# Optimization experiments

Measured on AMD Instinct MI355X. Metric: run time of the kernel, lower is better.

The kernel has to match this reference:

```python
import jax, jax.numpy as jnp
import numpy as np
from jax import lax

EPS = 1e-5
DN = ('NCHW', 'OIHW', 'NCHW')


def binarize(x):
    # sign(x) with 0 -> +1, matching _STESign.forward
    return jnp.where(x >= 0, jnp.ones_like(x), -jnp.ones_like(x))


def batchnorm(x, g, b, m, v):
    # inference BatchNorm2d with running stats
    scale = (g / jnp.sqrt(v + EPS))[None, :, None, None]
    shift = (b - m * g / jnp.sqrt(v + EPS))[None, :, None, None]
    return x * scale + shift


def conv(x, w, stride):
    return lax.conv_general_dilated(x, w, (stride, stride), [(1, 1), (1, 1)],
                                    dimension_numbers=DN)


def setup_inputs() -> dict:
    key = jax.random.key(0)
    ks = jax.random.split(key, 24)
    d = {}
    d['x'] = jax.random.normal(ks[0], (32, 3, 224, 224), dtype=jnp.float32)
    d['conv1_w'] = jax.random.normal(ks[1], (32, 3, 3, 3), dtype=jnp.float32) * 0.1
    d['conv2_w'] = jax.random.normal(ks[2], (64, 32, 3, 3), dtype=jnp.float32) * 0.1
    d['conv3_w'] = jax.random.normal(ks[3], (128, 64, 3, 3), dtype=jnp.float32) * 0.1
    d['conv4_w'] = jax.random.normal(ks[4], (256, 128, 3, 3), dtype=jnp.float32) * 0.1
    for i, c in zip(range(1, 5), (32, 64, 128, 256)):
        base = 4 + (i - 1) * 4
        d[f'bn{i}_g'] = jax.random.uniform(ks[base + 1], (c,), dtype=jnp.float32) + 0.5
        d[f'bn{i}_b'] = jax.random.normal(ks[base + 2], (c,), dtype=jnp.float32) * 0.1
        d[f'bn{i}_m'] = jax.random.normal(ks[base + 3], (c,), dtype=jnp.float32) * 0.1
        d[f'bn{i}_v'] = jax.random.uniform(ks[base + 4], (c,), dtype=jnp.float32) + 0.5
    d['fc_w'] = jax.random.normal(ks[21], (2, 256), dtype=jnp.float32) * 0.05
    d['fc_b'] = jnp.zeros((2,), dtype=jnp.float32)
    return d


def reference(x, conv1_w, conv2_w, conv3_w, conv4_w,
              bn1_g, bn1_b, bn1_m, bn1_v,
              bn2_g, bn2_b, bn2_m, bn2_v,
              bn3_g, bn3_b, bn3_m, bn3_v,
              bn4_g, bn4_b, bn4_m, bn4_v,
              fc_w, fc_b):
    # conv1 (real) + bn1
    h = batchnorm(conv(x, conv1_w, 1), bn1_g, bn1_b, bn1_m, bn1_v)
    # BinarizeConv2d: binarize input and weight, then real conv
    h = binarize(batchnorm(conv(binarize(h), binarize(conv2_w), 2), bn2_g, bn2_b, bn2_m, bn2_v))
    h = binarize(batchnorm(conv(binarize(h), binarize(conv3_w), 2), bn3_g, bn3_b, bn3_m, bn3_v))
    h = binarize(batchnorm(conv(binarize(h), binarize(conv4_w), 2), bn4_g, bn4_b, bn4_m, bn4_v))
    # adaptive avg pool to 1x1 -> mean over H,W
    h = jnp.mean(h, axis=(2, 3))  # [B, 256]
    return h @ fc_w.T + fc_b
```

## Files before the change

kernel.cpp:

```cpp
#include <hip/hip_runtime.h>
#include <stdint.h>
#include <math.h>

#define OFF_S1     0
#define OFF_W1T    256
#define OFF_T2     3712
#define OFF_P2     3968
#define OFF_T3     4224
#define OFF_P3     4736
#define OFF_T4     5248
#define OFF_P4     6272
#define OFF_W2     7296
#define OFF_W3     9600
#define OFF_W4     18816
#define OFF_A1     55680
#define OFF_A2     6478208
#define OFF_A3     9689472
#define OFF_A4     11295104

static __device__ __forceinline__ float2 bnf(float g, float b, float m, float v) {
    float sc = __fdiv_rn(g, __fsqrt_rn(__fadd_rn(v, 1e-5f)));
    float sh = __fsub_rn(b, __fmul_rn(m, sc));
    return make_float2(sc, sh);
}
static __device__ __forceinline__ bool bnpos(float s, float2 p) {
    return __fadd_rn(__fmul_rn(s, p.x), p.y) >= 0.0f;
}
static __device__ __forceinline__ int find_T(int K, float2 p) {
    int lo = -K - 2, hi = K + 2;
    while (lo + 2 < hi) {
        int mid = ((lo + hi) >> 1) & ~1;
        if (bnpos((float)mid, p)) hi = mid; else lo = mid;
    }
    return hi;
}

__global__ __launch_bounds__(256) void k_prep(
    const float* __restrict__ w1, const float* __restrict__ w2,
    const float* __restrict__ w3, const float* __restrict__ w4,
    const float* g1, const float* b1, const float* m1, const float* v1,
    const float* g2, const float* b2, const float* m2, const float* v2,
    const float* g3, const float* b3, const float* m3, const float* v3,
    const float* g4, const float* b4, const float* m4, const float* v4,
    float2* __restrict__ S1, float* __restrict__ W1T,
    int* __restrict__ T2, int* __restrict__ P2,
    int* __restrict__ T3, int* __restrict__ P3,
    int* __restrict__ T4, int* __restrict__ P4,
    uint32_t* __restrict__ W2, uint64_t* __restrict__ W3, uint64_t* __restrict__ W4)
{
    int gtid = blockIdx.x * 256 + threadIdx.x;
    int wid  = gtid >> 6;
    int lane = gtid & 63;

    if (wid < 576) {
        int oc = wid / 9, t = wid - oc * 9;
        float v = (lane < 32) ? w2[oc * 288 + lane * 9 + t] : -1.0f;
        uint64_t m = __ballot(v >= 0.0f);
        if (lane == 0) W2[wid] = (uint32_t)m;
    } else if (wid < 1728) {
        int i = wid - 576;
        int oc = i / 9, t = i - oc * 9;
        float v = w3[oc * 576 + lane * 9 + t];
        uint64_t m = __ballot(v >= 0.0f);
        if (lane == 0) W3[i] = m;
    } else if (wid < 6336) {
        int i = wid - 1728;
        int oc = i / 18, rem = i - oc * 18;
        int t = rem >> 1, h = rem & 1;
        float v = w4[oc * 1152 + (h * 64 + lane) * 9 + t];
        uint64_t m = __ballot(v >= 0.0f);
        if (lane == 0) W4[i] = m;
    } else {
        int t = gtid - 405504;
        if (t < 864) {
            int k = t >> 5, oc = t & 31;
            W1T[t] = w1[oc * 27 + k];
        } else if (t < 896) {
            int c = t - 864;
            S1[c] = bnf(g1[c], b1[c], m1[c], v1[c]);
        } else if (t < 960) {
            int c = t - 896;
            int T = find_T(288, bnf(g2[c], b2[c], m2[c], v2[c]));
            T2[c] = T; P2[c] = (288 - T) >> 1;
        } else if (t < 1088) {
            int c = t - 960;
            int T = find_T(576, bnf(g3[c], b3[c], m3[c], v3[c]));
            T3[c] = T; P3[c] = (576 - T) >> 1;
        } else if (t < 1344) {
            int c = t - 1088;
            int T = find_T(1152, bnf(g4[c], b4[c], m4[c], v4[c]));
            T4[c] = T; P4[c] = (1152 - T) >> 1;
        }
    }
}

__global__ __launch_bounds__(256) void k_conv1(
    const float* __restrict__ x, const float* __restrict__ w1,
    const float2* __restrict__ S1g, uint32_t* __restrict__ A1)
{
    __shared__ float  wl[27 * 32];
    __shared__ float2 s1[32];
    int tid = threadIdx.x;
    for (int i = tid; i < 864; i += 256) {
        int k = i >> 5, oc = i & 31;
        wl[i] = w1[oc * 27 + k];
    }
    if (tid < 32) s1[tid] = S1g[tid];
    __syncthreads();

    int idx = blockIdx.x * 256 + tid;
    int xp = idx % 112;
    int t  = idx / 112;
    int y  = t % 224;
    int b  = t / 224;
    int xc = xp * 2;

    const float* xb = x + (size_t)b * 3 * 50176;
    float xin[3][3][4];
    if ((unsigned)(y - 1) < 222u && (unsigned)(xp - 1) < 110u) {
        #pragma unroll
        for (int ic = 0; ic < 3; ic++)
            #pragma unroll
            for (int ky = 0; ky < 3; ky++) {
                const float* rp = xb + ic * 50176 + (y - 1 + ky) * 224 + (xc - 1);
                #pragma unroll
                for (int cx = 0; cx < 4; cx++) xin[ic][ky][cx] = rp[cx];
            }
    } else {
        #pragma unroll
        for (int ic = 0; ic < 3; ic++)
            #pragma unroll
            for (int ky = 0; ky < 3; ky++)
                #pragma unroll
                for (int cx = 0; cx < 4; cx++) {
                    int iy = y - 1 + ky, ix = xc - 1 + cx;
                    float v = 0.0f;
                    if ((unsigned)iy < 224u && (unsigned)ix < 224u)
                        v = xb[ic * 50176 + iy * 224 + ix];
                    xin[ic][ky][cx] = v;
                }
    }

    float acc0[32], acc1[32];
    #pragma unroll
    for (int oc = 0; oc < 32; oc++) { acc0[oc] = 0.0f; acc1[oc] = 0.0f; }

    const float4* wl4 = (const float4*)wl;
    #pragma unroll
    for (int k = 0; k < 27; k++) {
        int ic = k / 9, r = (k % 9) / 3, c = k % 3;
        float a0 = xin[ic][r][c];
        float a1 = xin[ic][r][c + 1];
        #pragma unroll
        for (int g8 = 0; g8 < 8; g8++) {
            float4 w = wl4[k * 8 + g8];
            acc0[g8 * 4 + 0] = fmaf(a0, w.x, acc0[g8 * 4 + 0]);
            acc0[g8 * 4 + 1] = fmaf(a0, w.y, acc0[g8 * 4 + 1]);
            acc0[g8 * 4 + 2] = fmaf(a0, w.z, acc0[g8 * 4 + 2]);
            acc0[g8 * 4 + 3] = fmaf(a0, w.w, acc0[g8 * 4 + 3]);
            acc1[g8 * 4 + 0] = fmaf(a1, w.x, acc1[g8 * 4 + 0]);
            acc1[g8 * 4 + 1] = fmaf(a1, w.y, acc1[g8 * 4 + 1]);
            acc1[g8 * 4 + 2] = fmaf(a1, w.z, acc1[g8 * 4 + 2]);
            acc1[g8 * 4 + 3] = fmaf(a1, w.w, acc1[g8 * 4 + 3]);
        }
    }

    uint32_t bits0 = 0, bits1 = 0;
    #pragma unroll
    for (int oc = 0; oc < 32; oc++) {
        bits0 |= (uint32_t)bnpos(acc0[oc], s1[oc]) << oc;
        bits1 |= (uint32_t)bnpos(acc1[oc], s1[oc]) << oc;
    }
    uint2* dst = (uint2*)(A1 + (size_t)b * 50176 + y * 224 + xc);
    *dst = make_uint2(bits0, bits1);
}

#define C2_LW 114
#define C3_LW 57

template<unsigned VM>
static __device__ __forceinline__ bool pred2(const uint32_t (&w)[3][9], int j,
                                             const uint32_t (&wr)[9], int T) {
    int pc = 0;
    #pragma unroll
    for (int ky = 0; ky < 3; ky++)
        #pragma unroll
        for (int kx = 0; kx < 3; kx++) {
            int ti = ky * 3 + kx;
            if (VM & (1u << ti)) pc += __popc(w[ky][2 * j + kx] ^ wr[ti]);
        }
    constexpr int nv = __builtin_popcount(VM);
    return pc <= ((32 * nv - T) >> 1);
}

template<unsigned VM0, unsigned VM>
static __device__ __forceinline__ void group2(const uint32_t* lrow, int g,
        const uint32_t (&wr)[9], int T, uint64_t* dst, int lane) {
    uint32_t win[3][9];
    int c0 = 8 * g;
    #pragma unroll
    for (int r = 0; r < 3; r++) {
        const uint32_t* rp = lrow + r * C2_LW + c0;
        uint2 a0 = *(const uint2*)(rp);
        uint2 a1 = *(const uint2*)(rp + 2);
        uint2 a2 = *(const uint2*)(rp + 4);
        uint2 a3 = *(const uint2*)(rp + 6);
        win[r][0] = a0.x; win[r][1] = a0.y; win[r][2] = a1.x; win[r][3] = a1.y;
        win[r][4] = a2.x; win[r][5] = a2.y; win[r][6] = a3.x; win[r][7] = a3.y;
        win[r][8] = rp[8];
    }
    uint64_t b0 = __ballot(pred2<VM0>(win, 0, wr, T));
    uint64_t b1 = __ballot(pred2<VM >(win, 1, wr, T));
    uint64_t b2 = __ballot(pred2<VM >(win, 2, wr, T));
    uint64_t b3 = __ballot(pred2<VM >(win, 3, wr, T));
    if (lane == 0) {
        ulonglong2* d = (ulonglong2*)(dst + 4 * g);
        d[0] = make_ulonglong2(b0, b1);
        d[1] = make_ulonglong2(b2, b3);
    }
}

__global__ __launch_bounds__(256) void k_conv2(
    const uint32_t* __restrict__ A1, const uint32_t* __restrict__ W2g,
    const int* __restrict__ T2, uint64_t* __restrict__ A2)
{
    __shared__ uint32_t lds[9 * C2_LW];
    int bi = blockIdx.x;
    int b = bi / 56, rem = bi % 56;
    int oyq = rem >> 1, h = rem & 1;
    int xs = h * 56;
    int tid = threadIdx.x;
    const uint32_t* ap = A1 + (size_t)b * 50176;
    for (int i = tid; i < 9 * C2_LW; i += 256) {
        int r = i / C2_LW, c = i - r * C2_LW;
        int iy = oyq * 8 - 1 + r, ix = 2 * xs - 1 + c;
        uint32_t v = 0;
        if ((unsigned)iy < 224u && (unsigned)ix < 224u) v = ap[iy * 224 + ix];
        lds[i] = v;
    }
    __syncthreads();

    int w = tid >> 6, lane = tid & 63;
    int oy = oyq * 4 + w;
    uint32_t wr[9];
    #pragma unroll
    for (int ti = 0; ti < 9; ti++) wr[ti] = W2g[lane * 9 + ti];
    int T = T2[lane];
    const uint32_t* lrow = lds + 2 * w * C2_LW;
    uint64_t* dst = A2 + (size_t)b * 12544 + oy * 112 + xs;
    bool left = (xs == 0);

    if (oy == 0) {
        if (left) group2<0x1B0, 0x1F8>(lrow, 0, wr, T, dst, lane);
        else      group2<0x1F8, 0x1F8>(lrow, 0, wr, T, dst, lane);
        for (int g = 1; g < 14; g++) group2<0x1F8, 0x1F8>(lrow, g, wr, T, dst, lane);
    } else {
        if (left) group2<0x1B6, 0x1FF>(lrow, 0, wr, T, dst, lane);
        else      group2<0x1FF, 0x1FF>(lrow, 0, wr, T, dst, lane);
        for (int g = 1; g < 14; g++) group2<0x1FF, 0x1FF>(lrow, g, wr, T, dst, lane);
    }
}

template<unsigned VM>
static __device__ __forceinline__ bool pred3(const uint64_t (&w)[3][9], int j,
                                             const uint64_t (&wr)[9], int T) {
    int pc = 0;
    #pragma unroll
    for (int ky = 0; ky < 3; ky++)
        #pragma unroll
        for (int kx = 0; kx < 3; kx++) {
            int ti = ky * 3 + kx;
            if (VM & (1u << ti)) pc += __popcll(w[ky][2 * j + kx] ^ wr[ti]);
        }
    constexpr int nv = __builtin_popcount(VM);
    return pc <= ((64 * nv - T) >> 1);
}

template<unsigned VM0, unsigned VM>
static __device__ __forceinline__ void group3(const uint64_t* lrow, int g,
        const uint64_t (&wr)[9], int T, uint64_t* dst, int lane) {
    uint64_t win[3][9];
    int c0 = 8 * g;
    #pragma unroll
    for (int r = 0; r < 3; r++) {
        const uint64_t* rp = lrow + r * C3_LW + c0;
        ulonglong2 a0 = *(const ulonglong2*)(rp);
        ulonglong2 a1 = *(const ulonglong2*)(rp + 2);
        ulonglong2 a2 = *(const ulonglong2*)(rp + 4);
        ulonglong2 a3 = *(const ulonglong2*)(rp + 6);
        win[r][0] = a0.x; win[r][1] = a0.y; win[r][2] = a1.x; win[r][3] = a1.y;
        win[r][4] = a2.x; win[r][5] = a2.y; win[r][6] = a3.x; win[r][7] = a3.y;
        win[r][8] = rp[8];
    }
    uint64_t b0 = __ballot(pred3<VM0>(win, 0, wr, T));
    uint64_t b1 = __ballot(pred3<VM >(win, 1, wr, T));
    uint64_t b2 = __ballot(pred3<VM >(win, 2, wr, T));
    uint64_t b3 = __ballot(pred3<VM >(win, 3, wr, T));
    if (lane == 0) {
        ulonglong2* d = (ulonglong2*)(dst + 4 * g);
        d[0] = make_ulonglong2(b0, b1);
        d[1] = make_ulonglong2(b2, b3);
    }
}

__global__ __launch_bounds__(256) void k_conv3(
    const uint64_t* __restrict__ A2, const uint64_t* __restrict__ W3g,
    const int* __restrict__ T3, uint64_t* __restrict__ A3)
{
    __shared__ uint64_t lds[5 * C3_LW];
    int bi = blockIdx.x;
    int b = bi / 56, rem = bi % 56;
    int oyp = rem >> 1, h = rem & 1;
    int xs = h * 28;
    int tid = threadIdx.x;
    const uint64_t* ap = A2 + (size_t)b * 12544;
    for (int i = tid; i < 5 * C3_LW; i += 256) {
        int r = i / C3_LW, c = i - r * C3_LW;
        int iy = oyp * 4 - 1 + r, ix = 2 * xs - 1 + c;
        uint64_t v = 0;
        if ((unsigned)iy < 112u && (unsigned)ix < 112u) v = ap[iy * 112 + ix];
        lds[i] = v;
    }
    __syncthreads();

    int w = tid >> 6, lane = tid & 63;
    int oy = oyp * 2 + (w >> 1);
    int g  = w & 1;
    int oc = g * 64 + lane;
    uint64_t wr[9];
    #pragma unroll
    for (int ti = 0; ti < 9; ti++) wr[ti] = W3g[oc * 9 + ti];
    int T = T3[oc];
    const uint64_t* lrow = lds + 2 * (w >> 1) * C3_LW;
    uint64_t* dst = A3 + (size_t)g * 100352 + (size_t)b * 3136 + oy * 56 + xs;
    bool left = (xs == 0);

    if (oy == 0) {
        if (left) group3<0x1B0, 0x1F8>(lrow, 0, wr, T, dst, lane);
        else      group3<0x1F8, 0x1F8>(lrow, 0, wr, T, dst, lane);
        for (int gg = 1; gg < 7; gg++) group3<0x1F8, 0x1F8>(lrow, gg, wr, T, dst, lane);
    } else {
        if (left) group3<0x1B6, 0x1FF>(lrow, 0, wr, T, dst, lane);
        else      group3<0x1FF, 0x1FF>(lrow, 0, wr, T, dst, lane);
        for (int gg = 1; gg < 7; gg++) group3<0x1FF, 0x1FF>(lrow, gg, wr, T, dst, lane);
    }
}

template<unsigned VM>
static __device__ __forceinline__ bool pred4(const uint64_t (&w0)[3][5],
                                             const uint64_t (&w1)[3][5], int j,
                                             const ulonglong2 (&wr)[9], int T) {
    int pc = 0;
    #pragma unroll
    for (int ky = 0; ky < 3; ky++)
        #pragma unroll
        for (int kx = 0; kx < 3; kx++) {
            int ti = ky * 3 + kx;
            if (VM & (1u << ti)) {
                pc += __popcll(w0[ky][2 * j + kx] ^ wr[ti].x);
                pc += __popcll(w1[ky][2 * j + kx] ^ wr[ti].y);
            }
        }
    constexpr int nv = __builtin_popcount(VM);
    return pc <= ((128 * nv - T) >> 1);
}

template<unsigned VM0, unsigned VM>
static __device__ __forceinline__ void group4(const uint64_t* ldsb, int g,
        const ulonglong2 (&wr)[9], int T, uint64_t* dst, int lane) {
    uint64_t w0[3][5], w1[3][5];
    int c0 = 4 * g;
    #pragma unroll
    for (int r = 0; r < 3; r++) {
        const uint64_t* rp0 = ldsb + r * 30 + c0;
        const uint64_t* rp1 = ldsb + (3 + r) * 30 + c0;
        ulonglong2 a0 = *(const ulonglong2*)(rp0);
        ulonglong2 a1 = *(const ulonglong2*)(rp0 + 2);
        w0[r][0] = a0.x; w0[r][1] = a0.y; w0[r][2] = a1.x; w0[r][3] = a1.y;
        w0[r][4] = rp0[4];
        ulonglong2 b0 = *(const ulonglong2*)(rp1);
        ulonglong2 b1 = *(const ulonglong2*)(rp1 + 2);
        w1[r][0] = b0.x; w1[r][1] = b0.y; w1[r][2] = b1.x; w1[r][3] = b1.y;
        w1[r][4] = rp1[4];
    }
    uint64_t r0 = __ballot(pred4<VM0>(w0, w1, 0, wr, T));
    uint64_t r1 = __ballot(pred4<VM >(w0, w1, 1, wr, T));
    if (lane == 0)
        *(ulonglong2*)(dst + 2 * g) = make_ulonglong2(r0, r1);
}

__global__ __launch_bounds__(256) void k_conv4(
    const uint64_t* __restrict__ A3, const uint64_t* __restrict__ W4g,
    const int* __restrict__ T4, uint64_t* __restrict__ A4)
{
    __shared__ uint64_t lds[2 * 3 * 30];
    int bi = blockIdx.x;
    int b = bi / 56, rem = bi % 56;
    int oy = rem >> 1, h = rem & 1;
    int xs = h * 14;
    int tid = threadIdx.x;
    const uint64_t* ap = A3 + (size_t)b * 3136;
    for (int i = tid; i < 174; i += 256) {
        int p = i / 87, j = i - p * 87;
        int r = j / 29, c = j - r * 29;
        int iy = 2 * oy - 1 + r, ix = 2 * xs - 1 + c;
        uint64_t v = 0;
        if ((unsigned)iy < 56u && (unsigned)ix < 56u)
            v = ap[(size_t)p * 100352 + iy * 56 + ix];
        lds[(p * 3 + r) * 30 + c] = v;
    }
    __syncthreads();

    int w = tid >> 6, lane = tid & 63;
    int oc = w * 64 + lane;
    ulonglong2 wr[9];
    const ulonglong2* wp = (const ulonglong2*)(W4g + oc * 18);
    #pragma unroll
    for (int ti = 0; ti < 9; ti++) wr[ti] = wp[ti];
    int T = T4[oc];
    uint64_t* dst = A4 + (size_t)w * 25088 + (size_t)b * 784 + oy * 28 + xs;
    bool left = (xs == 0);

    if (oy == 0) {
        if (left) group4<0x1B0, 0x1F8>(lds, 0, wr, T, dst, lane);
        else      group4<0x1F8, 0x1F8>(lds, 0, wr, T, dst, lane);
        for (int g = 1; g < 7; g++) group4<0x1F8, 0x1F8>(lds, g, wr, T, dst, lane);
    } else {
        if (left) group4<0x1B6, 0x1FF>(lds, 0, wr, T, dst, lane);
        else      group4<0x1FF, 0x1FF>(lds, 0, wr, T, dst, lane);
        for (int g = 1; g < 7; g++) group4<0x1FF, 0x1FF>(lds, g, wr, T, dst, lane);
    }
}

__global__ __launch_bounds__(1024) void k_tail(
    const uint64_t* __restrict__ A4, const float* __restrict__ fcw,
    const float* __restrict__ fcb, float* __restrict__ out)
{
    int b = blockIdx.x;
    int tid = threadIdx.x;
    int c = tid & 255, chunk = tid >> 8;
    int g = c >> 6, bit = c & 63;
    const uint64_t* base = A4 + (size_t)g * 25088 + (size_t)b * 784 + chunk * 196;
    const ulonglong2* bp = (const ulonglong2*)base;
    int cnt = 0;
    for (int i = 0; i < 98; i++) {
        ulonglong2 v = bp[i];
        cnt += (int)((v.x >> bit) & 1ull) + (int)((v.y >> bit) & 1ull);
    }

    __shared__ int cnts[4][256];
    __shared__ double r0[256], r1[256];
    cnts[chunk][c] = cnt;
    __syncthreads();
    if (tid < 256) {
        int tot = cnts[0][c] + cnts[1][c] + cnts[2][c] + cnts[3][c];
        double mean = (2.0 * (double)tot - 784.0) * (1.0 / 784.0);
        r0[c] = (double)fcw[c]       * mean;
        r1[c] = (double)fcw[256 + c] * mean;
    }
    __syncthreads();
    for (int s = 128; s > 0; s >>= 1) {
        if (tid < s) { r0[tid] += r0[tid + s]; r1[tid] += r1[tid + s]; }
        __syncthreads();
    }
    if (tid == 0) {
        out[b * 2 + 0] = (float)(r0[0] + (double)fcb[0]);
        out[b * 2 + 1] = (float)(r1[0] + (double)fcb[1]);
    }
}

extern "C" void kernel_launch(void* const* d_in, const int* in_sizes, int n_in,
                              void* d_out, int out_size, void* d_ws, size_t ws_size,
                              hipStream_t stream) {
    const float* x   = (const float*)d_in[0];
    const float* w1  = (const float*)d_in[1];
    const float* w2  = (const float*)d_in[2];
    const float* w3  = (const float*)d_in[3];
    const float* w4  = (const float*)d_in[4];
    const float* g1 = (const float*)d_in[5],  *b1 = (const float*)d_in[6],
               * m1 = (const float*)d_in[7],  *v1 = (const float*)d_in[8];
    const float* g2 = (const float*)d_in[9],  *b2 = (const float*)d_in[10],
               * m2 = (const float*)d_in[11], *v2 = (const float*)d_in[12];
    const float* g3 = (const float*)d_in[13], *b3 = (const float*)d_in[14],
               * m3 = (const float*)d_in[15], *v3 = (const float*)d_in[16];
    const float* g4 = (const float*)d_in[17], *b4 = (const float*)d_in[18],
               * m4 = (const float*)d_in[19], *v4 = (const float*)d_in[20];
    const float* fcw = (const float*)d_in[21];
    const float* fcb = (const float*)d_in[22];
    float* out = (float*)d_out;

    char* ws = (char*)d_ws;
    float2*   S1  = (float2*)(ws + OFF_S1);
    float*    W1T = (float*)(ws + OFF_W1T);
    int*      T2  = (int*)(ws + OFF_T2);
    int*      P2  = (int*)(ws + OFF_P2);
    int*      T3  = (int*)(ws + OFF_T3);
    int*      P3  = (int*)(ws + OFF_P3);
    int*      T4  = (int*)(ws + OFF_T4);
    int*      P4  = (int*)(ws + OFF_P4);
    uint32_t* W2  = (uint32_t*)(ws + OFF_W2);
    uint64_t* W3  = (uint64_t*)(ws + OFF_W3);
    uint64_t* W4  = (uint64_t*)(ws + OFF_W4);
    uint32_t* A1  = (uint32_t*)(ws + OFF_A1);
    uint64_t* A2  = (uint64_t*)(ws + OFF_A2);
    uint64_t* A3  = (uint64_t*)(ws + OFF_A3);
    uint64_t* A4  = (uint64_t*)(ws + OFF_A4);

    hipLaunchKernelGGL(k_prep, dim3(1590), dim3(256), 0, stream,
                       w1, w2, w3, w4,
                       g1, b1, m1, v1, g2, b2, m2, v2,
                       g3, b3, m3, v3, g4, b4, m4, v4,
                       S1, W1T, T2, P2, T3, P3, T4, P4, W2, W3, W4);
    hipLaunchKernelGGL(k_conv1, dim3(3136), dim3(256), 0, stream, x, w1, S1, A1);
    hipLaunchKernelGGL(k_conv2, dim3(1792), dim3(256), 0, stream, A1, W2, T2, A2);
    hipLaunchKernelGGL(k_conv3, dim3(1792), dim3(256), 0, stream, A2, W3, T3, A3);
    hipLaunchKernelGGL(k_conv4, dim3(1792), dim3(256), 0, stream, A3, W4, T4, A4);
    hipLaunchKernelGGL(k_tail,  dim3(32),   dim3(1024), 0, stream, A4, fcw, fcb, out);
}
```

Before: 244.7 us.

## Fuse weight prep into conv1 launch and compute four outputs per thread

Merges the weight-binarization/threshold prep kernel and conv1 into one launch, with extra blocks doing the prep and conv1 computing its BN scale inline. Each conv1 thread now produces four adjacent pixels instead of two, reusing a 6-wide input row and each shared weight load across more FMAs, and writes one 16-byte store. LDS row pitches in conv2/conv3 are padded and aligned so window loads can use 16-byte vector reads. The cost is higher register pressure from 128 accumulators, which may lower occupancy.

Measured after the change: 281.7 us. +15.1%, slower.

```diff
diff --git a/kernel.cpp b/kernel.cpp
--- a/kernel.cpp
+++ b/kernel.cpp
@@ -2,14 +2,9 @@
 #include <stdint.h>
 #include <math.h>
 
-#define OFF_S1     0
-#define OFF_W1T    256
 #define OFF_T2     3712
-#define OFF_P2     3968
 #define OFF_T3     4224
-#define OFF_P3     4736
 #define OFF_T4     5248
-#define OFF_P4     6272
 #define OFF_W2     7296
 #define OFF_W3     9600
 #define OFF_W4     18816
@@ -35,148 +30,144 @@
     return hi;
 }
 
-__global__ __launch_bounds__(256) void k_prep(
-    const float* __restrict__ w1, const float* __restrict__ w2,
-    const float* __restrict__ w3, const float* __restrict__ w4,
-    const float* g1, const float* b1, const float* m1, const float* v1,
+#define CONV1_BLOCKS 1568
+#define PREP_BLOCKS  1586
+
+__global__ __launch_bounds__(256) void k_front(
+    const float* __restrict__ x, const float* __restrict__ w1,
+    const float* __restrict__ g1, const float* __restrict__ b1,
+    const float* __restrict__ m1, const float* __restrict__ v1,
+    const float* __restrict__ w2, const float* __restrict__ w3, const float* __restrict__ w4,
     const float* g2, const float* b2, const float* m2, const float* v2,
     const float* g3, const float* b3, const float* m3, const float* v3,
     const float* g4, const float* b4, const float* m4, const float* v4,
-    float2* __restrict__ S1, float* __restrict__ W1T,
-    int* __restrict__ T2, int* __restrict__ P2,
-    int* __restrict__ T3, int* __restrict__ P3,
-    int* __restrict__ T4, int* __restrict__ P4,
+    uint32_t* __restrict__ A1,
+    int* __restrict__ T2, int* __restrict__ T3, int* __restrict__ T4,
     uint32_t* __restrict__ W2, uint64_t* __restrict__ W3, uint64_t* __restrict__ W4)
 {
-    int gtid = blockIdx.x * 256 + threadIdx.x;
-    int wid  = gtid >> 6;
-    int lane = gtid & 63;
-
-    if (wid < 576) {
-        int oc = wid / 9, t = wid - oc * 9;
-        float v = (lane < 32) ? w2[oc * 288 + lane * 9 + t] : -1.0f;
-        uint64_t m = __ballot(v >= 0.0f);
-        if (lane == 0) W2[wid] = (uint32_t)m;
-    } else if (wid < 1728) {
-        int i = wid - 576;
-        int oc = i / 9, t = i - oc * 9;
-        float v = w3[oc * 576 + lane * 9 + t];
-        uint64_t m = __ballot(v >= 0.0f);
-        if (lane == 0) W3[i] = m;
-    } else if (wid < 6336) {
-        int i = wid - 1728;
-        int oc = i / 18, rem = i - oc * 18;
-        int t = rem >> 1, h = rem & 1;
-        float v = w4[oc * 1152 + (h * 64 + lane) * 9 + t];
-        uint64_t m = __ballot(v >= 0.0f);
-        if (lane == 0) W4[i] = m;
-    } else {
-        int t = gtid - 405504;
-        if (t < 864) {
-            int k = t >> 5, oc = t & 31;
-            W1T[t] = w1[oc * 27 + k];
-        } else if (t < 896) {
-            int c = t - 864;
-            S1[c] = bnf(g1[c], b1[c], m1[c], v1[c]);
-        } else if (t < 960) {
-            int c = t - 896;
-            int T = find_T(288, bnf(g2[c], b2[c], m2[c], v2[c]));
-            T2[c] = T; P2[c] = (288 - T) >> 1;
-        } else if (t < 1088) {
-            int c = t - 960;
-            int T = find_T(576, bnf(g3[c], b3[c], m3[c], v3[c]));
-            T3[c] = T; P3[c] = (576 - T) >> 1;
-        } else if (t < 1344) {
-            int c = t - 1088;
-            int T = find_T(1152, bnf(g4[c], b4[c], m4[c], v4[c]));
-            T4[c] = T; P4[c] = (1152 - T) >> 1;
+    int tid = threadIdx.x;
+    if (blockIdx.x >= CONV1_BLOCKS) {
+        int gtid = (blockIdx.x - CONV1_BLOCKS) * 256 + tid;
+        int wid  = gtid >> 6;
+        int lane = gtid & 63;
+        if (wid < 576) {
+            int oc = wid / 9, t = wid - oc * 9;
+            float v = (lane < 32) ? w2[oc * 288 + lane * 9 + t] : -1.0f;
+            uint64_t m = __ballot(v >= 0.0f);
+            if (lane == 0) W2[wid] = (uint32_t)m;
+        } else if (wid < 1728) {
+            int i = wid - 576;
+            int oc = i / 9, t = i - oc * 9;
+            float v = w3[oc * 576 + lane * 9 + t];
+            uint64_t m = __ballot(v >= 0.0f);
+            if (lane == 0) W3[i] = m;
+        } else if (wid < 6336) {
+            int i = wid - 1728;
+            int oc = i / 18, rem = i - oc * 18;
+            int t = rem >> 1, h = rem & 1;
+            float v = w4[oc * 1152 + (h * 64 + lane) * 9 + t];
+            uint64_t m = __ballot(v >= 0.0f);
+            if (lane == 0) W4[i] = m;
+        } else {
+            int c = (wid - 6336) * 64 + lane;
+            if (c < 64) {
+                T2[c] = find_T(288, bnf(g2[c], b2[c], m2[c], v2[c]));
+            } else if (c < 192) {
+                int cc = c - 64;
+                T3[cc] = find_T(576, bnf(g3[cc], b3[cc], m3[cc], v3[cc]));
+            } else if (c < 448) {
+                int cc = c - 192;
+                T4[cc] = find_T(1152, bnf(g4[cc], b4[cc], m4[cc], v4[cc]));
+            }
         }
-    }
-}
-
-__global__ __launch_bounds__(256) void k_conv1(
-    const float* __restrict__ x, const float* __restrict__ w1,
-    const float2* __restrict__ S1g, uint32_t* __restrict__ A1)
-{
+        return;
+    }
+
     __shared__ float  wl[27 * 32];
     __shared__ float2 s1[32];
-    int tid = threadIdx.x;
     for (int i = tid; i < 864; i += 256) {
         int k = i >> 5, oc = i & 31;
         wl[i] = w1[oc * 27 + k];
     }
-    if (tid < 32) s1[tid] = S1g[tid];
+    if (tid < 32) s1[tid] = bnf(g1[tid], b1[tid], m1[tid], v1[tid]);
     __syncthreads();
 
     int idx = blockIdx.x * 256 + tid;
-    int xp = idx % 112;
-    int t  = idx / 112;
+    int xq = idx % 56;
+    int t  = idx / 56;
     int y  = t % 224;
     int b  = t / 224;
-    int xc = xp * 2;
+    int xc = xq * 4;
 
     const float* xb = x + (size_t)b * 3 * 50176;
-    float xin[3][3][4];
-    if ((unsigned)(y - 1) < 222u && (unsigned)(xp - 1) < 110u) {
+    bool xok = ((unsigned)(xq - 1) < 54u);
+
+    float acc0[32], acc1[32], acc2[32], acc3[32];
+    #pragma unroll
+    for (int oc = 0; oc < 32; oc++) {
+        acc0[oc] = 0.0f; acc1[oc] = 0.0f; acc2[oc] = 0.0f; acc3[oc] = 0.0f;
+    }
+
+    const float4* wl4 = (const float4*)wl;
+    for (int ic = 0; ic < 3; ic++) {
         #pragma unroll
-        for (int ic = 0; ic < 3; ic++)
+        for (int ky = 0; ky < 3; ky++) {
+            int iy = y - 1 + ky;
+            float r[6];
+            const float* rp = xb + ic * 50176 + iy * 224 + (xc - 1);
+            if (xok && (unsigned)iy < 224u) {
+                #pragma unroll
+                for (int c = 0; c < 6; c++) r[c] = rp[c];
+            } else {
+                #pragma unroll
+                for (int c = 0; c < 6; c++) {
+                    int ix = xc - 1 + c;
+                    r[c] = ((unsigned)iy < 224u && (unsigned)ix < 224u) ? rp[c] : 0.0f;
+                }
+            }
             #pragma unroll
-            for (int ky = 0; ky < 3; ky++) {
-                const float* rp = xb + ic * 50176 + (y - 1 + ky) * 224 + (xc - 1);
+            for (int kx = 0; kx < 3; kx++) {
+                int k = ic * 9 + ky * 3 + kx;
+                float a0 = r[kx], a1 = r[kx + 1], a2 = r[kx + 2], a3 = r[kx + 3];
                 #pragma unroll
-                for (int cx = 0; cx < 4; cx++) xin[ic][ky][cx] = rp[cx];
+                for (int g8 = 0; g8 < 8; g8++) {
+                    float4 w = wl4[k * 8 + g8];
+                    acc0[g8*4+0] = fmaf(a0, w.x, acc0[g8*4+0]);
+                    acc0[g8*4+1] = fmaf(a0, w.y, acc0[g8*4+1]);
+                    acc0[g8*4+2] = fmaf(a0, w.z, acc0[g8*4+2]);
+                    acc0[g8*4+3] = fmaf(a0, w.w, acc0[g8*4+3]);
+                    acc1[g8*4+0] = fmaf(a1, w.x, acc1[g8*4+0]);
+                    acc1[g8*4+1] = fmaf(a1, w.y, acc1[g8*4+1]);
+                    acc1[g8*4+2] = fmaf(a1, w.z, acc1[g8*4+2]);
+                    acc1[g8*4+3] = fmaf(a1, w.w, acc1[g8*4+3]);
+                    acc2[g8*4+0] = fmaf(a2, w.x, acc2[g8*4+0]);
+                    acc2[g8*4+1] = fmaf(a2, w.y, acc2[g8*4+1]);
+                    acc2[g8*4+2] = fmaf(a2, w.z, acc2[g8*4+2]);
+                    acc2[g8*4+3] = fmaf(a2, w.w, acc2[g8*4+3]);
+                    acc3[g8*4+0] = fmaf(a3, w.x, acc3[g8*4+0]);
+                    acc3[g8*4+1] = fmaf(a3, w.y, acc3[g8*4+1]);
+                    acc3[g8*4+2] = fmaf(a3, w.z, acc3[g8*4+2]);
+                    acc3[g8*4+3] = fmaf(a3, w.w, acc3[g8*4+3]);
+                }
             }
-    } else {
-        #pragma unroll
-        for (int ic = 0; ic < 3; ic++)
-            #pragma unroll
-            for (int ky = 0; ky < 3; ky++)
-                #pragma unroll
-                for (int cx = 0; cx < 4; cx++) {
-                    int iy = y - 1 + ky, ix = xc - 1 + cx;
-                    float v = 0.0f;
-                    if ((unsigned)iy < 224u && (unsigned)ix < 224u)
-                        v = xb[ic * 50176 + iy * 224 + ix];
-                    xin[ic][ky][cx] = v;
-                }
-    }
-
-    float acc0[32], acc1[32];
-    #pragma unroll
-    for (int oc = 0; oc < 32; oc++) { acc0[oc] = 0.0f; acc1[oc] = 0.0f; }
-
-    const float4* wl4 = (const float4*)wl;
-    #pragma unroll
-    for (int k = 0; k < 27; k++) {
-        int ic = k / 9, r = (k % 9) / 3, c = k % 3;
-        float a0 = xin[ic][r][c];
-        float a1 = xin[ic][r][c + 1];
-        #pragma unroll
-        for (int g8 = 0; g8 < 8; g8++) {
-            float4 w = wl4[k * 8 + g8];
-            acc0[g8 * 4 + 0] = fmaf(a0, w.x, acc0[g8 * 4 + 0]);
-            acc0[g8 * 4 + 1] = fmaf(a0, w.y, acc0[g8 * 4 + 1]);
-            acc0[g8 * 4 + 2] = fmaf(a0, w.z, acc0[g8 * 4 + 2]);
-            acc0[g8 * 4 + 3] = fmaf(a0, w.w, acc0[g8 * 4 + 3]);
-            acc1[g8 * 4 + 0] = fmaf(a1, w.x, acc1[g8 * 4 + 0]);
-            acc1[g8 * 4 + 1] = fmaf(a1, w.y, acc1[g8 * 4 + 1]);
-            acc1[g8 * 4 + 2] = fmaf(a1, w.z, acc1[g8 * 4 + 2]);
-            acc1[g8 * 4 + 3] = fmaf(a1, w.w, acc1[g8 * 4 + 3]);
         }
     }
 
-    uint32_t bits0 = 0, bits1 = 0;
+    uint32_t bits0 = 0, bits1 = 0, bits2 = 0, bits3 = 0;
     #pragma unroll
     for (int oc = 0; oc < 32; oc++) {
-        bits0 |= (uint32_t)bnpos(acc0[oc], s1[oc]) << oc;
-        bits1 |= (uint32_t)bnpos(acc1[oc], s1[oc]) << oc;
-    }
-    uint2* dst = (uint2*)(A1 + (size_t)b * 50176 + y * 224 + xc);
-    *dst = make_uint2(bits0, bits1);
-}
-
-#define C2_LW 114
-#define C3_LW 57
+        float2 p = s1[oc];
+        bits0 |= (uint32_t)bnpos(acc0[oc], p) << oc;
+        bits1 |= (uint32_t)bnpos(acc1[oc], p) << oc;
+        bits2 |= (uint32_t)bnpos(acc2[oc], p) << oc;
+        bits3 |= (uint32_t)bnpos(acc3[oc], p) << oc;
+    }
+    uint4* dst = (uint4*)(A1 + (size_t)b * 50176 + y * 224 + xc);
+    *dst = make_uint4(bits0, bits1, bits2, bits3);
+}
+
+#define C2_LW 116
+#define C3_LW 58
 
 template<unsigned VM>
 static __device__ __forceinline__ bool pred2(const uint32_t (&w)[3][9], int j,
@@ -201,12 +192,10 @@
     #pragma unroll
     for (int r = 0; r < 3; r++) {
         const uint32_t* rp = lrow + r * C2_LW + c0;
-        uint2 a0 = *(const uint2*)(rp);
-        uint2 a1 = *(const uint2*)(rp + 2);
-        uint2 a2 = *(const uint2*)(rp + 4);
-        uint2 a3 = *(const uint2*)(rp + 6);
-        win[r][0] = a0.x; win[r][1] = a0.y; win[r][2] = a1.x; win[r][3] = a1.y;
-        win[r][4] = a2.x; win[r][5] = a2.y; win[r][6] = a3.x; win[r][7] = a3.y;
+        uint4 a = *(const uint4*)(rp);
+        uint4 b = *(const uint4*)(rp + 4);
+        win[r][0] = a.x; win[r][1] = a.y; win[r][2] = a.z; win[r][3] = a.w;
+        win[r][4] = b.x; win[r][5] = b.y; win[r][6] = b.z; win[r][7] = b.w;
         win[r][8] = rp[8];
     }
     uint64_t b0 = __ballot(pred2<VM0>(win, 0, wr, T));
@@ -224,7 +213,7 @@
     const uint32_t* __restrict__ A1, const uint32_t* __restrict__ W2g,
     const int* __restrict__ T2, uint64_t* __restrict__ A2)
 {
-    __shared__ uint32_t lds[9 * C2_LW];
+    __shared__ __align__(16) uint32_t lds[9 * C2_LW];
     int bi = blockIdx.x;
     int b = bi / 56, rem = bi % 56;
     int oyq = rem >> 1, h = rem & 1;
@@ -307,7 +296,7 @@
     const uint64_t* __restrict__ A2, const uint64_t* __restrict__ W3g,
     const int* __restrict__ T3, uint64_t* __restrict__ A3)
 {
-    __shared__ uint64_t lds[5 * C3_LW];
+    __shared__ __align__(16) uint64_t lds[5 * C3_LW];
     int bi = blockIdx.x;
     int b = bi / 56, rem = bi % 56;
     int oyp = rem >> 1, h = rem & 1;
@@ -393,7 +382,7 @@
     const uint64_t* __restrict__ A3, const uint64_t* __restrict__ W4g,
     const int* __restrict__ T4, uint64_t* __restrict__ A4)
 {
-    __shared__ uint64_t lds[2 * 3 * 30];
+    __shared__ __align__(16) uint64_t lds[2 * 3 * 30];
     int bi = blockIdx.x;
     int b = bi / 56, rem = bi % 56;
     int oy = rem >> 1, h = rem & 1;
@@ -490,14 +479,9 @@
     float* out = (float*)d_out;
 
     char* ws = (char*)d_ws;
-    float2*   S1  = (float2*)(ws + OFF_S1);
-    float*    W1T = (float*)(ws + OFF_W1T);
     int*      T2  = (int*)(ws + OFF_T2);
-    int*      P2  = (int*)(ws + OFF_P2);
     int*      T3  = (int*)(ws + OFF_T3);
-    int*      P3  = (int*)(ws + OFF_P3);
     int*      T4  = (int*)(ws + OFF_T4);
-    int*      P4  = (int*)(ws + OFF_P4);
     uint32_t* W2  = (uint32_t*)(ws + OFF_W2);
     uint64_t* W3  = (uint64_t*)(ws + OFF_W3);
     uint64_t* W4  = (uint64_t*)(ws + OFF_W4);
@@ -506,12 +490,10 @@
     uint64_t* A3  = (uint64_t*)(ws + OFF_A3);
     uint64_t* A4  = (uint64_t*)(ws + OFF_A4);
 
-    hipLaunchKernelGGL(k_prep, dim3(1590), dim3(256), 0, stream,
-                       w1, w2, w3, w4,
-                       g1, b1, m1, v1, g2, b2, m2, v2,
-                       g3, b3, m3, v3, g4, b4, m4, v4,
-                       S1, W1T, T2, P2, T3, P3, T4, P4, W2, W3, W4);
-    hipLaunchKernelGGL(k_conv1, dim3(3136), dim3(256), 0, stream, x, w1, S1, A1);
+    hipLaunchKernelGGL(k_front, dim3(CONV1_BLOCKS + PREP_BLOCKS), dim3(256), 0, stream,
+                       x, w1, g1, b1, m1, v1, w2, w3, w4,
+                       g2, b2, m2, v2, g3, b3, m3, v3, g4, b4, m4, v4,
+                       A1, T2, T3, T4, W2, W3, W4);
     hipLaunchKernelGGL(k_conv2, dim3(1792), dim3(256), 0, stream, A1, W2, T2, A2);
     hipLaunchKernelGGL(k_conv3, dim3(1792), dim3(256), 0, stream, A2, W3, T3, A3);
     hipLaunchKernelGGL(k_conv4, dim3(1792), dim3(256), 0, stream, A3, W4, T4, A4);
```
